# Optimization experiments

Hardware: AMD Instinct MI355X
Metric: run time of the kernel (lower is better)

The kernel has to match this reference:

```python
import jax, jax.numpy as jnp
import numpy as np

N_NODES = 512
STATE_DIM = 16
MESSAGE_DIM = 32
HID_MSG = 64
HID_RO = 64
N_STEPS = 5


def setup_inputs() -> dict:
    key = jax.random.key(0)
    ks = jax.random.split(key, 16)
    s, m, hm, hr = STATE_DIM, MESSAGE_DIM, HID_MSG, HID_RO
    gru_in = s + m
    k_gru = 1.0 / np.sqrt(s)
    inp = {
        'J': jax.random.normal(ks[0], (N_NODES, N_NODES), jnp.float32),
        'b': jax.random.normal(ks[1], (N_NODES,), jnp.float32),
        # message MLP (torch init: weight ~ N(0, 0.1), bias = 0)
        'W1': 0.1 * jax.random.normal(ks[2], (hm, 2 * s + 3), jnp.float32),
        'b1': jnp.zeros((hm,), jnp.float32),
        'W2': 0.1 * jax.random.normal(ks[3], (hm, hm), jnp.float32),
        'b2': jnp.zeros((hm,), jnp.float32),
        'W3': 0.1 * jax.random.normal(ks[4], (m, hm), jnp.float32),
        'b3': jnp.zeros((m,), jnp.float32),
        # GRUCell params (torch default: U(-1/sqrt(hidden), 1/sqrt(hidden)))
        'W_ih': jax.random.uniform(ks[5], (3 * s, gru_in), jnp.float32, -k_gru, k_gru),
        'b_ih': jnp.zeros((3 * s,), jnp.float32),
        'W_hh': jax.random.uniform(ks[6], (3 * s, s), jnp.float32, -k_gru, k_gru),
        'b_hh': jnp.zeros((3 * s,), jnp.float32),
        # readout MLP
        'Wr1': 0.1 * jax.random.normal(ks[7], (hr, s), jnp.float32),
        'br1': jnp.zeros((hr,), jnp.float32),
        'Wr2': 0.1 * jax.random.normal(ks[8], (hr, hr), jnp.float32),
        'br2': jnp.zeros((hr,), jnp.float32),
        'Wr3': 0.1 * jax.random.normal(ks[9], (2, hr), jnp.float32),
        'br3': jnp.zeros((2,), jnp.float32),
    }
    return inp


def _gru_cell(x, h, W_ih, b_ih, W_hh, b_hh):
    s = h.shape[-1]
    gi = x @ W_ih.T + b_ih  # (n, 3s)
    gh = h @ W_hh.T + b_hh  # (n, 3s)
    ir, iz, in_ = gi[:, :s], gi[:, s:2 * s], gi[:, 2 * s:]
    hr, hz, hn = gh[:, :s], gh[:, s:2 * s], gh[:, 2 * s:]
    r = jax.nn.sigmoid(ir + hr)
    z = jax.nn.sigmoid(iz + hz)
    n = jnp.tanh(in_ + r * hn)
    return (1.0 - z) * n + z * h


def reference(J, b, W1, b1, W2, b2, W3, b3, W_ih, b_ih, W_hh, b_hh,
              Wr1, br1, Wr2, br2, Wr3, br3):
    n = J.shape[0]
    s = W_hh.shape[1]
    # Split first message-MLP layer by input blocks [h_i | h_j | J_ij | b_i | b_j]
    # so we never materialize the (n, n, 2s+3) feature tensor.
    W1_hi = W1[:, :s]            # (hm, s)
    W1_hj = W1[:, s:2 * s]       # (hm, s)
    w_J = W1[:, 2 * s]           # (hm,)
    w_bi = W1[:, 2 * s + 1]      # (hm,)
    w_bj = W1[:, 2 * s + 2]      # (hm,)
    # static per-pair part of layer-1 preactivation: (n, n, hm)
    static1 = (J[:, :, None] * w_J
               + b[:, None, None] * w_bi
               + b[None, :, None] * w_bj
               + b1)

    h0 = jnp.zeros((n, s), jnp.float32)

    def step(h, _):
        pre = (h @ W1_hi.T)[:, None, :] + (h @ W1_hj.T)[None, :, :] + static1
        x = jax.nn.relu(pre)                      # (n, n, hm)
        x = jax.nn.relu(x @ W2.T + b2)            # (n, n, hm)
        msg = x @ W3.T + b3                       # (n, n, m)
        m_j = msg.sum(axis=0)                     # sum over i -> (n, m)
        gru_in = jnp.concatenate([h, m_j], axis=1)
        h_new = _gru_cell(gru_in, h, W_ih, b_ih, W_hh, b_hh)
        return h_new, None

    h, _ = jax.lax.scan(step, h0, None, length=N_STEPS)

    y = jax.nn.relu(h @ Wr1.T + br1)
    y = jax.nn.relu(y @ Wr2.T + br2)
    y = jax.nn.sigmoid(y @ Wr3.T + br3)           # (n, 2)
    y = y / jnp.sum(y, axis=1, keepdims=True)
    return y
```

## Files before the change

### kernel.cpp

```cpp
#include <hip/hip_runtime.h>
#include <hip/hip_bf16.h>

#define NN 512
#define NSTEPS 5

typedef __attribute__((ext_vector_type(8))) short short8;
typedef __attribute__((ext_vector_type(4))) float floatx4;

static __device__ __forceinline__ unsigned short f2bf(float f) {
    union { float f; unsigned u; } x; x.f = f;
    unsigned r = x.u + 0x7fffu + ((x.u >> 16) & 1u);
    return (unsigned short)(r >> 16);
}

static __device__ __forceinline__ unsigned pk2bf(float a, float b) {
    __hip_bfloat162 h = __float22bfloat162_rn(make_float2(a, b));
    return *reinterpret_cast<unsigned*>(&h);
}

__global__ void init_kernel(const float* __restrict__ J, const float* __restrict__ b,
                            const float* __restrict__ W1, const float* __restrict__ b1,
                            const float* __restrict__ W2,
                            float* __restrict__ Jt, float* __restrict__ aG, float* __restrict__ cG,
                            float* __restrict__ h0, float* __restrict__ wJ,
                            float* __restrict__ wbi, float* __restrict__ wbj,
                            float* __restrict__ W1hiT, float* __restrict__ W1hjT,
                            unsigned short* __restrict__ W2bf)
{
    int bx = blockIdx.x, tid = threadIdx.x;
    if (bx < 64) {
        __shared__ float tile[64][65];
        int ti = bx >> 3, tj = bx & 7;
        for (int p = 0; p < 16; ++p) {
            int e = p*256 + tid; int r = e >> 6, c = e & 63;
            tile[r][c] = J[(ti*64 + r)*512 + tj*64 + c];
        }
        __syncthreads();
        for (int p = 0; p < 16; ++p) {
            int e = p*256 + tid; int r = e >> 6, c = e & 63;
            Jt[(tj*64 + r)*512 + ti*64 + c] = tile[c][r];
        }
    } else if (bx < 96) {
        int gid = (bx - 64)*256 + tid;
        for (int p = 0; p < 4; ++p) {
            int idx = p*8192 + gid;
            int i = idx >> 6, o = idx & 63;
            aG[idx] = b[i] * W1[o*35 + 33];
        }
    } else if (bx < 128) {
        int gid = (bx - 96)*256 + tid;
        for (int p = 0; p < 4; ++p) {
            int idx = p*8192 + gid;
            int i = idx >> 6, o = idx & 63;
            cG[idx] = b[i] * W1[o*35 + 34] + b1[o];
        }
    } else if (bx == 128) {
        for (int p = 0; p < 16; ++p) {
            int flat = p*256 + tid;
            int jj = flat & 7;
            int lane = (flat >> 3) & 63;
            int tk = flat >> 9;
            int nt = tk >> 1, ks = tk & 1;
            int n = nt*16 + (lane & 15);
            int k = ks*32 + (lane >> 4)*8 + jj;
            W2bf[flat] = f2bf(W2[n*64 + k]);
        }
        if (tid < 64) {
            wJ[tid]  = W1[tid*35 + 32];
            wbi[tid] = W1[tid*35 + 33];
            wbj[tid] = W1[tid*35 + 34];
            #pragma unroll
            for (int s = 0; s < 16; ++s) {
                W1hiT[tid*16 + s] = W1[tid*35 + s];
                W1hjT[tid*16 + s] = W1[tid*35 + 16 + s];
            }
        }
    } else {
        for (int p = 0; p < 32; ++p) h0[p*256 + tid] = 0.f;
    }
}

__global__ __launch_bounds__(256) void edge_kernel(
    const float* __restrict__ Jt,
    const float* __restrict__ aIn, const float* __restrict__ cIn, const float* __restrict__ hIn,
    float* __restrict__ aOut, float* __restrict__ cOut, float* __restrict__ hOut,
    const unsigned short* __restrict__ W2bf, const float* __restrict__ wJ,
    const float* __restrict__ b2, const float* __restrict__ W3, const float* __restrict__ b3,
    const float* __restrict__ W_ih, const float* __restrict__ b_ih,
    const float* __restrict__ W_hh, const float* __restrict__ b_hh,
    const float* __restrict__ W1hiT, const float* __restrict__ W1hjT,
    const float* __restrict__ wbi, const float* __restrict__ wbj,
    const float* __restrict__ bvec, const float* __restrict__ b1,
    const float* __restrict__ Wr1, const float* __restrict__ br1,
    const float* __restrict__ Wr2, const float* __restrict__ br2,
    const float* __restrict__ Wr3, const float* __restrict__ br3,
    float* __restrict__ out, int last)
{
    const int j = blockIdx.x;
    const int tid = threadIdx.x;
    const int l = tid & 63, w = tid >> 6;
    const int m = l & 15, q = l >> 4;

    __shared__ float smWave[4][64];
    __shared__ float smMacc[64];
    __shared__ float smGin[48];
    __shared__ float smGi[48], smGh[48];
    __shared__ float smH[16];
    __shared__ float smY[64];
    __shared__ float smR[2];

    const floatx4* c4 = (const floatx4*)cIn;
    const floatx4* w4 = (const floatx4*)wJ;
    floatx4 cva = c4[j*16 + q*2],     cvb = c4[j*16 + q*2 + 1];
    floatx4 cvc = c4[j*16 + 8 + q*2], cvd = c4[j*16 + 8 + q*2 + 1];
    floatx4 wva = w4[q*2], wvb = w4[q*2+1], wvc = w4[8+q*2], wvd = w4[8+q*2+1];

    short8 bfw[4][2];
    {
        const short8* wb = (const short8*)W2bf;
        #pragma unroll
        for (int nt = 0; nt < 4; ++nt)
            #pragma unroll
            for (int ks = 0; ks < 2; ++ks)
                bfw[nt][ks] = wb[(nt*2 + ks)*64 + l];
    }
    float b2n[4];
    #pragma unroll
    for (int nt = 0; nt < 4; ++nt) b2n[nt] = b2[nt*16 + m];

    floatx4 acc[4];
    #pragma unroll
    for (int nt = 0; nt < 4; ++nt) acc[nt] = (floatx4){0.f,0.f,0.f,0.f};

    const floatx4* a4 = (const floatx4*)aIn;

    for (int c8 = 0; c8 < 8; ++c8) {
        int i = w*128 + c8*16 + m;
        float Jij = Jt[j*512 + i];
        floatx4 av0 = a4[i*16 + q*2],     av1 = a4[i*16 + q*2 + 1];
        floatx4 av2 = a4[i*16 + 8 + q*2], av3 = a4[i*16 + 8 + q*2 + 1];
        floatx4 x0, x1, x2, x3;
        #pragma unroll
        for (int e = 0; e < 4; ++e) {
            x0[e] = fmaxf(fmaf(Jij, wva[e], av0[e]) + cva[e], 0.f);
            x1[e] = fmaxf(fmaf(Jij, wvb[e], av1[e]) + cvb[e], 0.f);
            x2[e] = fmaxf(fmaf(Jij, wvc[e], av2[e]) + cvc[e], 0.f);
            x3[e] = fmaxf(fmaf(Jij, wvd[e], av3[e]) + cvd[e], 0.f);
        }
        union { short8 s; unsigned u[4]; } fa0, fa1;
        fa0.u[0] = pk2bf(x0[0], x0[1]); fa0.u[1] = pk2bf(x0[2], x0[3]);
        fa0.u[2] = pk2bf(x1[0], x1[1]); fa0.u[3] = pk2bf(x1[2], x1[3]);
        fa1.u[0] = pk2bf(x2[0], x2[1]); fa1.u[1] = pk2bf(x2[2], x2[3]);
        fa1.u[2] = pk2bf(x3[0], x3[1]); fa1.u[3] = pk2bf(x3[2], x3[3]);
        #pragma unroll
        for (int nt = 0; nt < 4; ++nt) {
            floatx4 d = {0.f,0.f,0.f,0.f};
            d = __builtin_amdgcn_mfma_f32_16x16x32_bf16(fa0.s, bfw[nt][0], d, 0, 0, 0);
            d = __builtin_amdgcn_mfma_f32_16x16x32_bf16(fa1.s, bfw[nt][1], d, 0, 0, 0);
            #pragma unroll
            for (int r = 0; r < 4; ++r)
                acc[nt][r] += fmaxf(d[r] + b2n[nt], 0.f);
        }
    }

    #pragma unroll
    for (int nt = 0; nt < 4; ++nt) {
        float v = acc[nt][0] + acc[nt][1] + acc[nt][2] + acc[nt][3];
        v += __shfl_xor(v, 16);
        v += __shfl_xor(v, 32);
        if (l < 16) smWave[w][nt*16 + l] = v;
    }
    if (tid < 16) smGin[tid] = hIn[j*16 + tid];
    __syncthreads();
    if (tid < 64) smMacc[tid] = smWave[0][tid] + smWave[1][tid] + smWave[2][tid] + smWave[3][tid];
    __syncthreads();

    {
        int o = tid >> 3, p = tid & 7;
        const floatx4* W3v = (const floatx4*)W3;
        floatx4 wv0 = W3v[o*16 + p*2], wv1 = W3v[o*16 + p*2 + 1];
        float part = 0.f;
        #pragma unroll
        for (int e = 0; e < 4; ++e) {
            part = fmaf(wv0[e], smMacc[p*8 + e], part);
            part = fmaf(wv1[e], smMacc[p*8 + 4 + e], part);
        }
        part += __shfl_xor(part, 1);
        part += __shfl_xor(part, 2);
        part += __shfl_xor(part, 4);
        if (p == 0) smGin[16 + o] = part + 512.f * b3[o];
    }
    __syncthreads();

    if (tid < 192) {
        int o = tid >> 2, p = tid & 3;
        const floatx4* Wv = (const floatx4*)W_ih;
        floatx4 w0 = Wv[o*12 + p*3], w1 = Wv[o*12 + p*3 + 1], w2 = Wv[o*12 + p*3 + 2];
        int k0 = p*12;
        float part = 0.f;
        #pragma unroll
        for (int e = 0; e < 4; ++e) {
            part = fmaf(w0[e], smGin[k0 + e], part);
            part = fmaf(w1[e], smGin[k0 + 4 + e], part);
            part = fmaf(w2[e], smGin[k0 + 8 + e], part);
        }
        part += __shfl_xor(part, 1);
        part += __shfl_xor(part, 2);
        if (p == 0) smGi[o] = part + b_ih[o];
    } else if (tid < 240) {
        int o = tid - 192;
        const floatx4* Wv = (const floatx4*)W_hh;
        floatx4 w0 = Wv[o*4], w1 = Wv[o*4+1], w2 = Wv[o*4+2], w3 = Wv[o*4+3];
        float s = b_hh[o];
        #pragma unroll
        for (int e = 0; e < 4; ++e) {
            s = fmaf(w0[e], smGin[e],      s);
            s = fmaf(w1[e], smGin[4 + e],  s);
            s = fmaf(w2[e], smGin[8 + e],  s);
            s = fmaf(w3[e], smGin[12 + e], s);
        }
        smGh[o] = s;
    }
    __syncthreads();

    if (tid < 16) {
        float r = 1.f / (1.f + __expf(-(smGi[tid] + smGh[tid])));
        float z = 1.f / (1.f + __expf(-(smGi[16+tid] + smGh[16+tid])));
        float n = tanhf(smGi[32+tid] + r * smGh[32+tid]);
        float hn = (1.f - z)*n + z*smGin[tid];
        hOut[j*16 + tid] = hn;
        smH[tid] = hn;
    }
    __syncthreads();

    if (!last) {
        if (tid < 128) {
            int o = tid & 63, sel = tid >> 6;
            const floatx4* Wv = (const floatx4*)(sel ? W1hjT : W1hiT);
            floatx4 w0 = Wv[o*4], w1 = Wv[o*4+1], w2 = Wv[o*4+2], w3 = Wv[o*4+3];
            float s = 0.f;
            #pragma unroll
            for (int e = 0; e < 4; ++e) {
                s = fmaf(w0[e], smH[e],      s);
                s = fmaf(w1[e], smH[4 + e],  s);
                s = fmaf(w2[e], smH[8 + e],  s);
                s = fmaf(w3[e], smH[12 + e], s);
            }
            if (sel == 0) aOut[j*64 + o] = s + bvec[j]*wbi[o];
            else          cOut[j*64 + o] = s + bvec[j]*wbj[o] + b1[o];
        }
    } else {
        if (tid < 64) {
            const floatx4* Wv = (const floatx4*)Wr1;
            floatx4 w0 = Wv[tid*4], w1 = Wv[tid*4+1], w2 = Wv[tid*4+2], w3 = Wv[tid*4+3];
            float s = br1[tid];
            #pragma unroll
            for (int e = 0; e < 4; ++e) {
                s = fmaf(w0[e], smH[e],      s);
                s = fmaf(w1[e], smH[4 + e],  s);
                s = fmaf(w2[e], smH[8 + e],  s);
                s = fmaf(w3[e], smH[12 + e], s);
            }
            smY[tid] = fmaxf(s, 0.f);
        }
        __syncthreads();
        {
            int o = tid >> 2, p = tid & 3;
            const floatx4* Wv = (const floatx4*)Wr2;
            floatx4 w0 = Wv[o*16 + p*4],     w1 = Wv[o*16 + p*4 + 1];
            floatx4 w2 = Wv[o*16 + p*4 + 2], w3 = Wv[o*16 + p*4 + 3];
            int k0 = p*16;
            float part = 0.f;
            #pragma unroll
            for (int e = 0; e < 4; ++e) {
                part = fmaf(w0[e], smY[k0 + e],      part);
                part = fmaf(w1[e], smY[k0 + 4 + e],  part);
                part = fmaf(w2[e], smY[k0 + 8 + e],  part);
                part = fmaf(w3[e], smY[k0 + 12 + e], part);
            }
            part += __shfl_xor(part, 1);
            part += __shfl_xor(part, 2);
            __syncthreads();
            if (p == 0) smY[o] = fmaxf(part + br2[o], 0.f);
        }
        __syncthreads();
        if (tid < 128) {
            int ot = tid >> 6, p = tid & 63;
            float part = Wr3[ot*64 + p] * smY[p];
            part += __shfl_xor(part, 1);
            part += __shfl_xor(part, 2);
            part += __shfl_xor(part, 4);
            part += __shfl_xor(part, 8);
            part += __shfl_xor(part, 16);
            part += __shfl_xor(part, 32);
            if (p == 0) smR[ot] = part + br3[ot];
        }
        __syncthreads();
        if (tid == 0) {
            float e0 = 1.f/(1.f + __expf(-smR[0]));
            float e1 = 1.f/(1.f + __expf(-smR[1]));
            float t = e0 + e1;
            out[j*2]     = e0/t;
            out[j*2 + 1] = e1/t;
        }
    }
}

extern "C" void kernel_launch(void* const* d_in, const int* in_sizes, int n_in,
                              void* d_out, int out_size, void* d_ws, size_t ws_size,
                              hipStream_t stream)
{
    const float* J    = (const float*)d_in[0];
    const float* b    = (const float*)d_in[1];
    const float* W1   = (const float*)d_in[2];
    const float* b1   = (const float*)d_in[3];
    const float* W2   = (const float*)d_in[4];
    const float* b2   = (const float*)d_in[5];
    const float* W3   = (const float*)d_in[6];
    const float* b3   = (const float*)d_in[7];
    const float* W_ih = (const float*)d_in[8];
    const float* b_ih = (const float*)d_in[9];
    const float* W_hh = (const float*)d_in[10];
    const float* b_hh = (const float*)d_in[11];
    const float* Wr1  = (const float*)d_in[12];
    const float* br1  = (const float*)d_in[13];
    const float* Wr2  = (const float*)d_in[14];
    const float* br2  = (const float*)d_in[15];
    const float* Wr3  = (const float*)d_in[16];
    const float* br3  = (const float*)d_in[17];
    float* out = (float*)d_out;

    float* ws   = (float*)d_ws;
    float* Jt   = ws;
    float* aG0  = Jt + 262144;
    float* aG1  = aG0 + 32768;
    float* cG0  = aG1 + 32768;
    float* cG1  = cG0 + 32768;
    float* hA   = cG1 + 32768;
    float* hB   = hA + 8192;
    float* wJ   = hB + 8192;
    float* wbi  = wJ + 64;
    float* wbj  = wbi + 64;
    float* W1hiT = wbj + 64;
    float* W1hjT = W1hiT + 1024;
    unsigned short* W2bf = (unsigned short*)(W1hjT + 1024);

    hipLaunchKernelGGL(init_kernel, dim3(130), dim3(256), 0, stream,
                       J, b, W1, b1, W2, Jt, aG0, cG0, hA, wJ, wbi, wbj, W1hiT, W1hjT, W2bf);

    float* aIn = aG0; float* aOut = aG1;
    float* cIn = cG0; float* cOut = cG1;
    float* hI  = hA;  float* hO  = hB;
    for (int t = 0; t < NSTEPS; ++t) {
        hipLaunchKernelGGL(edge_kernel, dim3(512), dim3(256), 0, stream,
            Jt, aIn, cIn, hI, aOut, cOut, hO, W2bf, wJ, b2, W3, b3,
            W_ih, b_ih, W_hh, b_hh, W1hiT, W1hjT, wbi, wbj, b, b1,
            Wr1, br1, Wr2, br2, Wr3, br3, out, (t == NSTEPS-1) ? 1 : 0);
        float* tmp;
        tmp = aIn; aIn = aOut; aOut = tmp;
        tmp = cIn; cIn = cOut; cOut = tmp;
        tmp = hI;  hI  = hO;  hO  = tmp;
    }
}
```

Measured before the change: 155.0 us.

## Fuse init and all GNN steps into one cooperative persistent kernel with grid sync

Replaces the init kernel plus five per-step edge kernel launches with a single cooperative kernel of 256 blocks, each handling two destination nodes. Steps are separated by grid.sync(), so launch overhead and inter-kernel gaps go away. The J column, W2 weights in bf16 and the W1 slices now stay in registers or shared memory across all steps instead of being reloaded each launch, and the J transpose is dropped. The trade-off is the cost of grid-wide barriers and fewer blocks; the old multi-launch path remains as a fallback if the cooperative launch fails.

```diff
diff --git a/kernel.cpp b/kernel.cpp
--- a/kernel.cpp
+++ b/kernel.cpp
@@ -1,5 +1,8 @@
 #include <hip/hip_runtime.h>
 #include <hip/hip_bf16.h>
+#include <hip/hip_cooperative_groups.h>
+
+namespace cg = cooperative_groups;
 
 #define NN 512
 #define NSTEPS 5
@@ -16,6 +19,287 @@
 static __device__ __forceinline__ unsigned pk2bf(float a, float b) {
     __hip_bfloat162 h = __float22bfloat162_rn(make_float2(a, b));
     return *reinterpret_cast<unsigned*>(&h);
+}
+
+__global__ __launch_bounds__(512, 2) void fused2_kernel(
+    const float* __restrict__ J, const float* __restrict__ b,
+    const float* __restrict__ W1, const float* __restrict__ b1,
+    const float* __restrict__ W2, const float* __restrict__ b2,
+    const float* __restrict__ W3, const float* __restrict__ b3,
+    const float* __restrict__ W_ih, const float* __restrict__ b_ih,
+    const float* __restrict__ W_hh, const float* __restrict__ b_hh,
+    const float* __restrict__ Wr1, const float* __restrict__ br1,
+    const float* __restrict__ Wr2, const float* __restrict__ br2,
+    const float* __restrict__ Wr3, const float* __restrict__ br3,
+    float* __restrict__ aBuf0, float* __restrict__ aBuf1,
+    float* __restrict__ out)
+{
+    cg::grid_group grid = cg::this_grid();
+    const int tid = threadIdx.x;
+    const int nd = tid >> 8;
+    const int tl = tid & 255;
+    const int j  = blockIdx.x * 2 + nd;
+    const int l  = tid & 63, w4 = tl >> 6;
+    const int m  = l & 15,  q  = l >> 4;
+
+    __shared__ float smW1hi[64][16], smW1hj[64][16];
+    __shared__ float smC[2][64], smAbias[2][64], smCbias[2][64];
+    __shared__ float smWave[2][4][64], smMacc[2][64];
+    __shared__ float smGin[2][48], smGi[2][48], smGh[2][48];
+    __shared__ float smH[2][16], smY[2][64], smR[2][2];
+
+    if (tid < 64) {
+        const float* w1r = W1 + tid*35;
+        #pragma unroll
+        for (int s = 0; s < 16; ++s) {
+            smW1hi[tid][s] = w1r[s];
+            smW1hj[tid][s] = w1r[16 + s];
+        }
+    }
+    if (tid < 128) {
+        int nd0 = tid >> 6, o = tid & 63;
+        int j0 = blockIdx.x*2 + nd0;
+        float bj0 = b[j0];
+        const float* w1r = W1 + o*35;
+        float ab = bj0 * w1r[33];
+        smAbias[nd0][o] = ab;
+        float cb = bj0 * w1r[34] + b1[o];
+        smCbias[nd0][o] = cb;
+        smC[nd0][o] = cb;
+        aBuf0[j0*64 + o] = ab;
+    }
+    if (tid >= 128 && tid < 160) {
+        int nd0 = (tid - 128) >> 4, o = (tid - 128) & 15;
+        smH[nd0][o] = 0.f;
+    }
+
+    float Jr[8];
+    #pragma unroll
+    for (int c8 = 0; c8 < 8; ++c8)
+        Jr[c8] = J[(w4*128 + c8*16 + m)*512 + j];
+
+    floatx4 wva, wvb, wvc, wvd;
+    #pragma unroll
+    for (int e = 0; e < 4; ++e) {
+        wva[e] = W1[(q*8 + e)*35 + 32];
+        wvb[e] = W1[(q*8 + 4 + e)*35 + 32];
+        wvc[e] = W1[(32 + q*8 + e)*35 + 32];
+        wvd[e] = W1[(32 + q*8 + 4 + e)*35 + 32];
+    }
+
+    short8 bfw[4][2];
+    #pragma unroll
+    for (int nt = 0; nt < 4; ++nt) {
+        #pragma unroll
+        for (int ks = 0; ks < 2; ++ks) {
+            union { short8 s; unsigned short us[8]; } tpk;
+            int n = nt*16 + m;
+            #pragma unroll
+            for (int jj = 0; jj < 8; ++jj)
+                tpk.us[jj] = f2bf(W2[n*64 + ks*32 + q*8 + jj]);
+            bfw[nt][ks] = tpk.s;
+        }
+    }
+    float b2n[4];
+    #pragma unroll
+    for (int nt = 0; nt < 4; ++nt) b2n[nt] = b2[nt*16 + m];
+
+    grid.sync();
+
+    float* aIn = aBuf0;
+    float* aOut = aBuf1;
+
+    for (int t = 0; t < NSTEPS; ++t) {
+        const int last = (t == NSTEPS - 1);
+
+        floatx4 cva, cvb, cvc, cvd;
+        #pragma unroll
+        for (int e = 0; e < 4; ++e) {
+            cva[e] = smC[nd][q*8 + e];
+            cvb[e] = smC[nd][q*8 + 4 + e];
+            cvc[e] = smC[nd][32 + q*8 + e];
+            cvd[e] = smC[nd][32 + q*8 + 4 + e];
+        }
+
+        floatx4 acc[4];
+        #pragma unroll
+        for (int nt = 0; nt < 4; ++nt) acc[nt] = (floatx4){0.f,0.f,0.f,0.f};
+
+        const floatx4* a4 = (const floatx4*)aIn;
+
+        for (int c8 = 0; c8 < 8; ++c8) {
+            int i = w4*128 + c8*16 + m;
+            float Jij = Jr[c8];
+            floatx4 av0 = a4[i*16 + q*2],     av1 = a4[i*16 + q*2 + 1];
+            floatx4 av2 = a4[i*16 + 8 + q*2], av3 = a4[i*16 + 8 + q*2 + 1];
+            floatx4 x0, x1, x2, x3;
+            #pragma unroll
+            for (int e = 0; e < 4; ++e) {
+                x0[e] = fmaxf(fmaf(Jij, wva[e], av0[e]) + cva[e], 0.f);
+                x1[e] = fmaxf(fmaf(Jij, wvb[e], av1[e]) + cvb[e], 0.f);
+                x2[e] = fmaxf(fmaf(Jij, wvc[e], av2[e]) + cvc[e], 0.f);
+                x3[e] = fmaxf(fmaf(Jij, wvd[e], av3[e]) + cvd[e], 0.f);
+            }
+            union { short8 s; unsigned u[4]; } fa0, fa1;
+            fa0.u[0] = pk2bf(x0[0], x0[1]); fa0.u[1] = pk2bf(x0[2], x0[3]);
+            fa0.u[2] = pk2bf(x1[0], x1[1]); fa0.u[3] = pk2bf(x1[2], x1[3]);
+            fa1.u[0] = pk2bf(x2[0], x2[1]); fa1.u[1] = pk2bf(x2[2], x2[3]);
+            fa1.u[2] = pk2bf(x3[0], x3[1]); fa1.u[3] = pk2bf(x3[2], x3[3]);
+            #pragma unroll
+            for (int nt = 0; nt < 4; ++nt) {
+                floatx4 d = {0.f,0.f,0.f,0.f};
+                d = __builtin_amdgcn_mfma_f32_16x16x32_bf16(fa0.s, bfw[nt][0], d, 0, 0, 0);
+                d = __builtin_amdgcn_mfma_f32_16x16x32_bf16(fa1.s, bfw[nt][1], d, 0, 0, 0);
+                #pragma unroll
+                for (int r = 0; r < 4; ++r)
+                    acc[nt][r] += fmaxf(d[r] + b2n[nt], 0.f);
+            }
+        }
+
+        #pragma unroll
+        for (int nt = 0; nt < 4; ++nt) {
+            float v = acc[nt][0] + acc[nt][1] + acc[nt][2] + acc[nt][3];
+            v += __shfl_xor(v, 16);
+            v += __shfl_xor(v, 32);
+            if (l < 16) smWave[nd][w4][nt*16 + l] = v;
+        }
+        if (tl < 16) smGin[nd][tl] = smH[nd][tl];
+        __syncthreads();
+        if (tl < 64) smMacc[nd][tl] = smWave[nd][0][tl] + smWave[nd][1][tl]
+                                    + smWave[nd][2][tl] + smWave[nd][3][tl];
+        __syncthreads();
+
+        {
+            int o = tl >> 3, p = tl & 7;
+            const floatx4* W3v = (const floatx4*)W3;
+            floatx4 wv0 = W3v[o*16 + p*2], wv1 = W3v[o*16 + p*2 + 1];
+            float part = 0.f;
+            #pragma unroll
+            for (int e = 0; e < 4; ++e) {
+                part = fmaf(wv0[e], smMacc[nd][p*8 + e], part);
+                part = fmaf(wv1[e], smMacc[nd][p*8 + 4 + e], part);
+            }
+            part += __shfl_xor(part, 1);
+            part += __shfl_xor(part, 2);
+            part += __shfl_xor(part, 4);
+            if (p == 0) smGin[nd][16 + o] = part + 512.f * b3[o];
+        }
+        __syncthreads();
+
+        if (tl < 192) {
+            int o = tl >> 2, p = tl & 3;
+            const floatx4* Wv = (const floatx4*)W_ih;
+            floatx4 w0 = Wv[o*12 + p*3], w1 = Wv[o*12 + p*3 + 1], w2 = Wv[o*12 + p*3 + 2];
+            int k0 = p*12;
+            float part = 0.f;
+            #pragma unroll
+            for (int e = 0; e < 4; ++e) {
+                part = fmaf(w0[e], smGin[nd][k0 + e], part);
+                part = fmaf(w1[e], smGin[nd][k0 + 4 + e], part);
+                part = fmaf(w2[e], smGin[nd][k0 + 8 + e], part);
+            }
+            part += __shfl_xor(part, 1);
+            part += __shfl_xor(part, 2);
+            if (p == 0) smGi[nd][o] = part + b_ih[o];
+        } else if (tl < 240) {
+            int o = tl - 192;
+            const floatx4* Wv = (const floatx4*)W_hh;
+            floatx4 w0 = Wv[o*4], w1 = Wv[o*4+1], w2 = Wv[o*4+2], w3 = Wv[o*4+3];
+            float s2 = b_hh[o];
+            #pragma unroll
+            for (int e = 0; e < 4; ++e) {
+                s2 = fmaf(w0[e], smGin[nd][e],      s2);
+                s2 = fmaf(w1[e], smGin[nd][4 + e],  s2);
+                s2 = fmaf(w2[e], smGin[nd][8 + e],  s2);
+                s2 = fmaf(w3[e], smGin[nd][12 + e], s2);
+            }
+            smGh[nd][o] = s2;
+        }
+        __syncthreads();
+
+        if (tl < 16) {
+            float r = 1.f / (1.f + __expf(-(smGi[nd][tl] + smGh[nd][tl])));
+            float z = 1.f / (1.f + __expf(-(smGi[nd][16+tl] + smGh[nd][16+tl])));
+            float n = tanhf(smGi[nd][32+tl] + r * smGh[nd][32+tl]);
+            float hn = (1.f - z)*n + z*smGin[nd][tl];
+            smH[nd][tl] = hn;
+        }
+        __syncthreads();
+
+        if (!last) {
+            if (tl < 128) {
+                int o = tl & 63, sel = tl >> 6;
+                const floatx4* Wv = (const floatx4*)(sel ? &smW1hj[0][0] : &smW1hi[0][0]);
+                floatx4 w0 = Wv[o*4], w1 = Wv[o*4+1], w2 = Wv[o*4+2], w3 = Wv[o*4+3];
+                float s = 0.f;
+                #pragma unroll
+                for (int e = 0; e < 4; ++e) {
+                    s = fmaf(w0[e], smH[nd][e],      s);
+                    s = fmaf(w1[e], smH[nd][4 + e],  s);
+                    s = fmaf(w2[e], smH[nd][8 + e],  s);
+                    s = fmaf(w3[e], smH[nd][12 + e], s);
+                }
+                if (sel == 0) aOut[j*64 + o] = s + smAbias[nd][o];
+                else          smC[nd][o] = s + smCbias[nd][o];
+            }
+            grid.sync();
+            float* tmp = aIn; aIn = aOut; aOut = tmp;
+        } else {
+            if (tl < 64) {
+                const floatx4* Wv = (const floatx4*)Wr1;
+                floatx4 w0 = Wv[tl*4], w1 = Wv[tl*4+1], w2 = Wv[tl*4+2], w3 = Wv[tl*4+3];
+                float s = br1[tl];
+                #pragma unroll
+                for (int e = 0; e < 4; ++e) {
+                    s = fmaf(w0[e], smH[nd][e],      s);
+                    s = fmaf(w1[e], smH[nd][4 + e],  s);
+                    s = fmaf(w2[e], smH[nd][8 + e],  s);
+                    s = fmaf(w3[e], smH[nd][12 + e], s);
+                }
+                smY[nd][tl] = fmaxf(s, 0.f);
+            }
+            __syncthreads();
+            {
+                int o = tl >> 2, p = tl & 3;
+                const floatx4* Wv = (const floatx4*)Wr2;
+                floatx4 w0 = Wv[o*16 + p*4],     w1 = Wv[o*16 + p*4 + 1];
+                floatx4 w2 = Wv[o*16 + p*4 + 2], w3 = Wv[o*16 + p*4 + 3];
+                int k0 = p*16;
+                float part = 0.f;
+                #pragma unroll
+                for (int e = 0; e < 4; ++e) {
+                    part = fmaf(w0[e], smY[nd][k0 + e],      part);
+                    part = fmaf(w1[e], smY[nd][k0 + 4 + e],  part);
+                    part = fmaf(w2[e], smY[nd][k0 + 8 + e],  part);
+                    part = fmaf(w3[e], smY[nd][k0 + 12 + e], part);
+                }
+                part += __shfl_xor(part, 1);
+                part += __shfl_xor(part, 2);
+                __syncthreads();
+                if (p == 0) smY[nd][o] = fmaxf(part + br2[o], 0.f);
+            }
+            __syncthreads();
+            if (tl < 128) {
+                int ot = tl >> 6, p = tl & 63;
+                float part = Wr3[ot*64 + p] * smY[nd][p];
+                part += __shfl_xor(part, 1);
+                part += __shfl_xor(part, 2);
+                part += __shfl_xor(part, 4);
+                part += __shfl_xor(part, 8);
+                part += __shfl_xor(part, 16);
+                part += __shfl_xor(part, 32);
+                if (p == 0) smR[nd][ot] = part + br3[ot];
+            }
+            __syncthreads();
+            if (tl == 0) {
+                float e0 = 1.f/(1.f + __expf(-smR[nd][0]));
+                float e1 = 1.f/(1.f + __expf(-smR[nd][1]));
+                float tsum = e0 + e1;
+                out[j*2]     = e0/tsum;
+                out[j*2 + 1] = e1/tsum;
+            }
+        }
+    }
 }
 
 __global__ void init_kernel(const float* __restrict__ J, const float* __restrict__ b,
@@ -328,10 +612,35 @@
     const float* br2  = (const float*)d_in[15];
     const float* Wr3  = (const float*)d_in[16];
     const float* br3  = (const float*)d_in[17];
-    float* out = (float*)d_out;
-
-    float* ws   = (float*)d_ws;
-    float* Jt   = ws;
+    float* outp = (float*)d_out;
+
+    float* ws = (float*)d_ws;
+
+    static int coop_attr = -1;
+    if (coop_attr < 0) {
+        int v = 0;
+        if (hipDeviceGetAttribute(&v, hipDeviceAttributeCooperativeLaunch, 0) != hipSuccess) v = 0;
+        coop_attr = v;
+    }
+
+    float* aBuf0 = ws;
+    float* aBuf1 = ws + 32768;
+
+    hipError_t lerr = hipErrorUnknown;
+    if (coop_attr) {
+        void* args[] = {
+            (void*)&J, (void*)&b, (void*)&W1, (void*)&b1, (void*)&W2, (void*)&b2,
+            (void*)&W3, (void*)&b3, (void*)&W_ih, (void*)&b_ih, (void*)&W_hh, (void*)&b_hh,
+            (void*)&Wr1, (void*)&br1, (void*)&Wr2, (void*)&br2, (void*)&Wr3, (void*)&br3,
+            (void*)&aBuf0, (void*)&aBuf1, (void*)&outp
+        };
+        lerr = hipLaunchCooperativeKernel(reinterpret_cast<void*>(fused2_kernel),
+                                          dim3(NN/2), dim3(512), args, 0, stream);
+    }
+    if (lerr == hipSuccess) return;
+    (void)hipGetLastError();
+
+    float* Jt   = ws + 65536;
     float* aG0  = Jt + 262144;
     float* aG1  = aG0 + 32768;
     float* cG0  = aG1 + 32768;
@@ -355,7 +664,7 @@
         hipLaunchKernelGGL(edge_kernel, dim3(512), dim3(256), 0, stream,
             Jt, aIn, cIn, hI, aOut, cOut, hO, W2bf, wJ, b2, W3, b3,
             W_ih, b_ih, W_hh, b_hh, W1hiT, W1hjT, wbi, wbj, b, b1,
-            Wr1, br1, Wr2, br2, Wr3, br3, out, (t == NSTEPS-1) ? 1 : 0);
+            Wr1, br1, Wr2, br2, Wr3, br3, outp, (t == NSTEPS-1) ? 1 : 0);
         float* tmp;
         tmp = aIn; aIn = aOut; aOut = tmp;
         tmp = cIn; cIn = cOut; cOut = tmp;
```

Measured after the change: 304.0 us. +96.1%, slower.

## Fuse init and all GRU steps into one persistent kernel with flag sync

Applied to the files above, without the earlier changes.

Replaces the init kernel and the five per-step launches with a single persistent kernel of 256 blocks, each handling two nodes. Blocks exchange the per-node layer-1 'a' vectors through per-step global buffers and spin on padded per-node flags rather than relying on kernel boundaries. The c vector and hidden state stay in shared memory. J is read column-wise directly into registers instead of through a transpose, and W2 is converted to bf16 in every block. The aim is to remove launch overhead and the full grid barrier between steps. In exchange it relies on all 256 blocks being co-resident and on correct memory ordering for the flag spin-waits, and it adds polling cost plus redundant per-block weight preparation.

```diff
diff --git a/kernel.cpp b/kernel.cpp
--- a/kernel.cpp
+++ b/kernel.cpp
@@ -3,6 +3,7 @@
 
 #define NN 512
 #define NSTEPS 5
+#define FSTR 32
 
 typedef __attribute__((ext_vector_type(8))) short short8;
 typedef __attribute__((ext_vector_type(4))) float floatx4;
@@ -18,290 +19,319 @@
     return *reinterpret_cast<unsigned*>(&h);
 }
 
-__global__ void init_kernel(const float* __restrict__ J, const float* __restrict__ b,
-                            const float* __restrict__ W1, const float* __restrict__ b1,
-                            const float* __restrict__ W2,
-                            float* __restrict__ Jt, float* __restrict__ aG, float* __restrict__ cG,
-                            float* __restrict__ h0, float* __restrict__ wJ,
-                            float* __restrict__ wbi, float* __restrict__ wbj,
-                            float* __restrict__ W1hiT, float* __restrict__ W1hjT,
-                            unsigned short* __restrict__ W2bf)
-{
-    int bx = blockIdx.x, tid = threadIdx.x;
-    if (bx < 64) {
-        __shared__ float tile[64][65];
-        int ti = bx >> 3, tj = bx & 7;
-        for (int p = 0; p < 16; ++p) {
-            int e = p*256 + tid; int r = e >> 6, c = e & 63;
-            tile[r][c] = J[(ti*64 + r)*512 + tj*64 + c];
-        }
-        __syncthreads();
-        for (int p = 0; p < 16; ++p) {
-            int e = p*256 + tid; int r = e >> 6, c = e & 63;
-            Jt[(tj*64 + r)*512 + ti*64 + c] = tile[c][r];
-        }
-    } else if (bx < 96) {
-        int gid = (bx - 64)*256 + tid;
-        for (int p = 0; p < 4; ++p) {
-            int idx = p*8192 + gid;
-            int i = idx >> 6, o = idx & 63;
-            aG[idx] = b[i] * W1[o*35 + 33];
-        }
-    } else if (bx < 128) {
-        int gid = (bx - 96)*256 + tid;
-        for (int p = 0; p < 4; ++p) {
-            int idx = p*8192 + gid;
-            int i = idx >> 6, o = idx & 63;
-            cG[idx] = b[i] * W1[o*35 + 34] + b1[o];
-        }
-    } else if (bx == 128) {
-        for (int p = 0; p < 16; ++p) {
-            int flat = p*256 + tid;
-            int jj = flat & 7;
-            int lane = (flat >> 3) & 63;
-            int tk = flat >> 9;
-            int nt = tk >> 1, ks = tk & 1;
-            int n = nt*16 + (lane & 15);
-            int k = ks*32 + (lane >> 4)*8 + jj;
-            W2bf[flat] = f2bf(W2[n*64 + k]);
-        }
-        if (tid < 64) {
-            wJ[tid]  = W1[tid*35 + 32];
-            wbi[tid] = W1[tid*35 + 33];
-            wbj[tid] = W1[tid*35 + 34];
-            #pragma unroll
-            for (int s = 0; s < 16; ++s) {
-                W1hiT[tid*16 + s] = W1[tid*35 + s];
-                W1hjT[tid*16 + s] = W1[tid*35 + 16 + s];
-            }
-        }
-    } else {
-        for (int p = 0; p < 32; ++p) h0[p*256 + tid] = 0.f;
-    }
-}
-
-__global__ __launch_bounds__(256) void edge_kernel(
-    const float* __restrict__ Jt,
-    const float* __restrict__ aIn, const float* __restrict__ cIn, const float* __restrict__ hIn,
-    float* __restrict__ aOut, float* __restrict__ cOut, float* __restrict__ hOut,
-    const unsigned short* __restrict__ W2bf, const float* __restrict__ wJ,
-    const float* __restrict__ b2, const float* __restrict__ W3, const float* __restrict__ b3,
+__global__ __launch_bounds__(512, 2) void fused3_kernel(
+    const float* __restrict__ J, const float* __restrict__ b,
+    const float* __restrict__ W1, const float* __restrict__ b1,
+    const float* __restrict__ W2, const float* __restrict__ b2,
+    const float* __restrict__ W3, const float* __restrict__ b3,
     const float* __restrict__ W_ih, const float* __restrict__ b_ih,
     const float* __restrict__ W_hh, const float* __restrict__ b_hh,
-    const float* __restrict__ W1hiT, const float* __restrict__ W1hjT,
-    const float* __restrict__ wbi, const float* __restrict__ wbj,
-    const float* __restrict__ bvec, const float* __restrict__ b1,
     const float* __restrict__ Wr1, const float* __restrict__ br1,
     const float* __restrict__ Wr2, const float* __restrict__ br2,
     const float* __restrict__ Wr3, const float* __restrict__ br3,
-    float* __restrict__ out, int last)
+    float* __restrict__ aP, int* __restrict__ flag,
+    float* __restrict__ out)
 {
-    const int j = blockIdx.x;
     const int tid = threadIdx.x;
-    const int l = tid & 63, w = tid >> 6;
-    const int m = l & 15, q = l >> 4;
-
-    __shared__ float smWave[4][64];
-    __shared__ float smMacc[64];
-    __shared__ float smGin[48];
-    __shared__ float smGi[48], smGh[48];
-    __shared__ float smH[16];
-    __shared__ float smY[64];
-    __shared__ float smR[2];
-
-    const floatx4* c4 = (const floatx4*)cIn;
-    const floatx4* w4 = (const floatx4*)wJ;
-    floatx4 cva = c4[j*16 + q*2],     cvb = c4[j*16 + q*2 + 1];
-    floatx4 cvc = c4[j*16 + 8 + q*2], cvd = c4[j*16 + 8 + q*2 + 1];
-    floatx4 wva = w4[q*2], wvb = w4[q*2+1], wvc = w4[8+q*2], wvd = w4[8+q*2+1];
+    const int bid = blockIdx.x;
+    const int nd = tid >> 8;
+    const int tl = tid & 255;
+    const int j  = bid * 2 + nd;
+    const int l  = tid & 63, w4 = tl >> 6;
+    const int m  = l & 15,  q  = l >> 4;
+
+    __shared__ float smW1hi[64][16], smW1hj[64][16];
+    __shared__ float smC[2][64], smAbias[2][64], smCbias[2][64];
+    __shared__ float smWave[2][4][64], smMacc[2][64];
+    __shared__ float smGin[2][48], smGi[2][48], smGh[2][48];
+    __shared__ float smH[2][16], smY[2][64], smR[2][2];
+
+    __builtin_amdgcn_fence(__ATOMIC_ACQUIRE, "agent");
+
+    if (tid < 128) {
+        int nd0 = tid >> 6, o = tid & 63;
+        int j0 = bid*2 + nd0;
+        float bj0 = b[j0];
+        const float* w1r = W1 + o*35;
+        float ab = bj0 * w1r[33];
+        smAbias[nd0][o] = ab;
+        float cb = bj0 * w1r[34] + b1[o];
+        smCbias[nd0][o] = cb;
+        smC[nd0][o] = cb;
+        __hip_atomic_store(&aP[32768 + j0*64 + o], ab,
+                           __ATOMIC_RELAXED, __HIP_MEMORY_SCOPE_AGENT);
+    }
+    if (tid < 128) {
+        asm volatile("s_waitcnt vmcnt(0)" ::: "memory");
+        if ((tid & 63) == 0)
+            __hip_atomic_store(&flag[(bid*2 + (tid >> 6))*FSTR], 1,
+                               __ATOMIC_RELAXED, __HIP_MEMORY_SCOPE_AGENT);
+    }
+    if (tid >= 128 && tid < 160) {
+        int nd0 = (tid - 128) >> 4, o = (tid - 128) & 15;
+        smH[nd0][o] = 0.f;
+    }
+    if (tid < 64) {
+        const float* w1r = W1 + tid*35;
+        #pragma unroll
+        for (int s0 = 0; s0 < 16; ++s0) {
+            smW1hi[tid][s0] = w1r[s0];
+            smW1hj[tid][s0] = w1r[16 + s0];
+        }
+    }
+
+    float Jr[8];
+    #pragma unroll
+    for (int c8 = 0; c8 < 8; ++c8)
+        Jr[c8] = J[(w4*128 + c8*16 + m)*512 + j];
+
+    floatx4 wva, wvb, wvc, wvd;
+    #pragma unroll
+    for (int e = 0; e < 4; ++e) {
+        wva[e] = W1[(q*8 + e)*35 + 32];
+        wvb[e] = W1[(q*8 + 4 + e)*35 + 32];
+        wvc[e] = W1[(32 + q*8 + e)*35 + 32];
+        wvd[e] = W1[(32 + q*8 + 4 + e)*35 + 32];
+    }
 
     short8 bfw[4][2];
-    {
-        const short8* wb = (const short8*)W2bf;
-        #pragma unroll
-        for (int nt = 0; nt < 4; ++nt)
-            #pragma unroll
-            for (int ks = 0; ks < 2; ++ks)
-                bfw[nt][ks] = wb[(nt*2 + ks)*64 + l];
+    #pragma unroll
+    for (int nt = 0; nt < 4; ++nt) {
+        #pragma unroll
+        for (int ks = 0; ks < 2; ++ks) {
+            union { short8 s; unsigned short us[8]; } tpk;
+            int n = nt*16 + m;
+            #pragma unroll
+            for (int jj = 0; jj < 8; ++jj)
+                tpk.us[jj] = f2bf(W2[n*64 + ks*32 + q*8 + jj]);
+            bfw[nt][ks] = tpk.s;
+        }
     }
     float b2n[4];
     #pragma unroll
     for (int nt = 0; nt < 4; ++nt) b2n[nt] = b2[nt*16 + m];
 
-    floatx4 acc[4];
-    #pragma unroll
-    for (int nt = 0; nt < 4; ++nt) acc[nt] = (floatx4){0.f,0.f,0.f,0.f};
-
-    const floatx4* a4 = (const floatx4*)aIn;
-
-    for (int c8 = 0; c8 < 8; ++c8) {
-        int i = w*128 + c8*16 + m;
-        float Jij = Jt[j*512 + i];
-        floatx4 av0 = a4[i*16 + q*2],     av1 = a4[i*16 + q*2 + 1];
-        floatx4 av2 = a4[i*16 + 8 + q*2], av3 = a4[i*16 + 8 + q*2 + 1];
-        floatx4 x0, x1, x2, x3;
+    __syncthreads();
+
+    for (int t = 0; t < NSTEPS; ++t) {
+        const int last = (t == NSTEPS - 1);
+        const int s = t + 1;
+
+        floatx4 cva, cvb, cvc, cvd;
         #pragma unroll
         for (int e = 0; e < 4; ++e) {
-            x0[e] = fmaxf(fmaf(Jij, wva[e], av0[e]) + cva[e], 0.f);
-            x1[e] = fmaxf(fmaf(Jij, wvb[e], av1[e]) + cvb[e], 0.f);
-            x2[e] = fmaxf(fmaf(Jij, wvc[e], av2[e]) + cvc[e], 0.f);
-            x3[e] = fmaxf(fmaf(Jij, wvd[e], av3[e]) + cvd[e], 0.f);
-        }
-        union { short8 s; unsigned u[4]; } fa0, fa1;
-        fa0.u[0] = pk2bf(x0[0], x0[1]); fa0.u[1] = pk2bf(x0[2], x0[3]);
-        fa0.u[2] = pk2bf(x1[0], x1[1]); fa0.u[3] = pk2bf(x1[2], x1[3]);
-        fa1.u[0] = pk2bf(x2[0], x2[1]); fa1.u[1] = pk2bf(x2[2], x2[3]);
-        fa1.u[2] = pk2bf(x3[0], x3[1]); fa1.u[3] = pk2bf(x3[2], x3[3]);
+            cva[e] = smC[nd][q*8 + e];
+            cvb[e] = smC[nd][q*8 + 4 + e];
+            cvc[e] = smC[nd][32 + q*8 + e];
+            cvd[e] = smC[nd][32 + q*8 + 4 + e];
+        }
+
+        {
+            const int rbase = w4*128 + m;
+            for (;;) {
+                int f0 = __hip_atomic_load(&flag[(rbase +   0)*FSTR], __ATOMIC_RELAXED, __HIP_MEMORY_SCOPE_AGENT);
+                int f1 = __hip_atomic_load(&flag[(rbase +  16)*FSTR], __ATOMIC_RELAXED, __HIP_MEMORY_SCOPE_AGENT);
+                int f2 = __hip_atomic_load(&flag[(rbase +  32)*FSTR], __ATOMIC_RELAXED, __HIP_MEMORY_SCOPE_AGENT);
+                int f3 = __hip_atomic_load(&flag[(rbase +  48)*FSTR], __ATOMIC_RELAXED, __HIP_MEMORY_SCOPE_AGENT);
+                int f4 = __hip_atomic_load(&flag[(rbase +  64)*FSTR], __ATOMIC_RELAXED, __HIP_MEMORY_SCOPE_AGENT);
+                int f5 = __hip_atomic_load(&flag[(rbase +  80)*FSTR], __ATOMIC_RELAXED, __HIP_MEMORY_SCOPE_AGENT);
+                int f6 = __hip_atomic_load(&flag[(rbase +  96)*FSTR], __ATOMIC_RELAXED, __HIP_MEMORY_SCOPE_AGENT);
+                int f7 = __hip_atomic_load(&flag[(rbase + 112)*FSTR], __ATOMIC_RELAXED, __HIP_MEMORY_SCOPE_AGENT);
+                int mn = min(min(min(f0, f1), min(f2, f3)),
+                             min(min(f4, f5), min(f6, f7)));
+                if (mn >= s) break;
+                __builtin_amdgcn_s_sleep(1);
+            }
+        }
+        asm volatile("" ::: "memory");
+
+        floatx4 acc[4];
+        #pragma unroll
+        for (int nt = 0; nt < 4; ++nt) acc[nt] = (floatx4){0.f,0.f,0.f,0.f};
+
+        const floatx4* a4 = (const floatx4*)(aP + (size_t)s*32768);
+
+        for (int c8 = 0; c8 < 8; ++c8) {
+            int i = w4*128 + c8*16 + m;
+            float Jij = Jr[c8];
+            floatx4 av0 = a4[i*16 + q*2],     av1 = a4[i*16 + q*2 + 1];
+            floatx4 av2 = a4[i*16 + 8 + q*2], av3 = a4[i*16 + 8 + q*2 + 1];
+            floatx4 x0, x1, x2, x3;
+            #pragma unroll
+            for (int e = 0; e < 4; ++e) {
+                x0[e] = fmaxf(fmaf(Jij, wva[e], av0[e]) + cva[e], 0.f);
+                x1[e] = fmaxf(fmaf(Jij, wvb[e], av1[e]) + cvb[e], 0.f);
+                x2[e] = fmaxf(fmaf(Jij, wvc[e], av2[e]) + cvc[e], 0.f);
+                x3[e] = fmaxf(fmaf(Jij, wvd[e], av3[e]) + cvd[e], 0.f);
+            }
+            union { short8 s; unsigned u[4]; } fa0, fa1;
+            fa0.u[0] = pk2bf(x0[0], x0[1]); fa0.u[1] = pk2bf(x0[2], x0[3]);
+            fa0.u[2] = pk2bf(x1[0], x1[1]); fa0.u[3] = pk2bf(x1[2], x1[3]);
+            fa1.u[0] = pk2bf(x2[0], x2[1]); fa1.u[1] = pk2bf(x2[2], x2[3]);
+            fa1.u[2] = pk2bf(x3[0], x3[1]); fa1.u[3] = pk2bf(x3[2], x3[3]);
+            #pragma unroll
+            for (int nt = 0; nt < 4; ++nt) {
+                floatx4 d = {0.f,0.f,0.f,0.f};
+                d = __builtin_amdgcn_mfma_f32_16x16x32_bf16(fa0.s, bfw[nt][0], d, 0, 0, 0);
+                d = __builtin_amdgcn_mfma_f32_16x16x32_bf16(fa1.s, bfw[nt][1], d, 0, 0, 0);
+                #pragma unroll
+                for (int r = 0; r < 4; ++r)
+                    acc[nt][r] += fmaxf(d[r] + b2n[nt], 0.f);
+            }
+        }
+
         #pragma unroll
         for (int nt = 0; nt < 4; ++nt) {
-            floatx4 d = {0.f,0.f,0.f,0.f};
-            d = __builtin_amdgcn_mfma_f32_16x16x32_bf16(fa0.s, bfw[nt][0], d, 0, 0, 0);
-            d = __builtin_amdgcn_mfma_f32_16x16x32_bf16(fa1.s, bfw[nt][1], d, 0, 0, 0);
-            #pragma unroll
-            for (int r = 0; r < 4; ++r)
-                acc[nt][r] += fmaxf(d[r] + b2n[nt], 0.f);
-        }
-    }
-
-    #pragma unroll
-    for (int nt = 0; nt < 4; ++nt) {
-        float v = acc[nt][0] + acc[nt][1] + acc[nt][2] + acc[nt][3];
-        v += __shfl_xor(v, 16);
-        v += __shfl_xor(v, 32);
-        if (l < 16) smWave[w][nt*16 + l] = v;
-    }
-    if (tid < 16) smGin[tid] = hIn[j*16 + tid];
-    __syncthreads();
-    if (tid < 64) smMacc[tid] = smWave[0][tid] + smWave[1][tid] + smWave[2][tid] + smWave[3][tid];
-    __syncthreads();
-
-    {
-        int o = tid >> 3, p = tid & 7;
-        const floatx4* W3v = (const floatx4*)W3;
-        floatx4 wv0 = W3v[o*16 + p*2], wv1 = W3v[o*16 + p*2 + 1];
-        float part = 0.f;
-        #pragma unroll
-        for (int e = 0; e < 4; ++e) {
-            part = fmaf(wv0[e], smMacc[p*8 + e], part);
-            part = fmaf(wv1[e], smMacc[p*8 + 4 + e], part);
-        }
-        part += __shfl_xor(part, 1);
-        part += __shfl_xor(part, 2);
-        part += __shfl_xor(part, 4);
-        if (p == 0) smGin[16 + o] = part + 512.f * b3[o];
-    }
-    __syncthreads();
-
-    if (tid < 192) {
-        int o = tid >> 2, p = tid & 3;
-        const floatx4* Wv = (const floatx4*)W_ih;
-        floatx4 w0 = Wv[o*12 + p*3], w1 = Wv[o*12 + p*3 + 1], w2 = Wv[o*12 + p*3 + 2];
-        int k0 = p*12;
-        float part = 0.f;
-        #pragma unroll
-        for (int e = 0; e < 4; ++e) {
-            part = fmaf(w0[e], smGin[k0 + e], part);
-            part = fmaf(w1[e], smGin[k0 + 4 + e], part);
-            part = fmaf(w2[e], smGin[k0 + 8 + e], part);
-        }
-        part += __shfl_xor(part, 1);
-        part += __shfl_xor(part, 2);
-        if (p == 0) smGi[o] = part + b_ih[o];
-    } else if (tid < 240) {
-        int o = tid - 192;
-        const floatx4* Wv = (const floatx4*)W_hh;
-        floatx4 w0 = Wv[o*4], w1 = Wv[o*4+1], w2 = Wv[o*4+2], w3 = Wv[o*4+3];
-        float s = b_hh[o];
-        #pragma unroll
-        for (int e = 0; e < 4; ++e) {
-            s = fmaf(w0[e], smGin[e],      s);
-            s = fmaf(w1[e], smGin[4 + e],  s);
-            s = fmaf(w2[e], smGin[8 + e],  s);
-            s = fmaf(w3[e], smGin[12 + e], s);
-        }
-        smGh[o] = s;
-    }
-    __syncthreads();
-
-    if (tid < 16) {
-        float r = 1.f / (1.f + __expf(-(smGi[tid] + smGh[tid])));
-        float z = 1.f / (1.f + __expf(-(smGi[16+tid] + smGh[16+tid])));
-        float n = tanhf(smGi[32+tid] + r * smGh[32+tid]);
-        float hn = (1.f - z)*n + z*smGin[tid];
-        hOut[j*16 + tid] = hn;
-        smH[tid] = hn;
-    }
-    __syncthreads();
-
-    if (!last) {
-        if (tid < 128) {
-            int o = tid & 63, sel = tid >> 6;
-            const floatx4* Wv = (const floatx4*)(sel ? W1hjT : W1hiT);
-            floatx4 w0 = Wv[o*4], w1 = Wv[o*4+1], w2 = Wv[o*4+2], w3 = Wv[o*4+3];
-            float s = 0.f;
+            float v = acc[nt][0] + acc[nt][1] + acc[nt][2] + acc[nt][3];
+            v += __shfl_xor(v, 16);
+            v += __shfl_xor(v, 32);
+            if (l < 16) smWave[nd][w4][nt*16 + l] = v;
+        }
+        if (tl < 16) smGin[nd][tl] = smH[nd][tl];
+        __syncthreads();
+        if (tl < 64) smMacc[nd][tl] = smWave[nd][0][tl] + smWave[nd][1][tl]
+                                    + smWave[nd][2][tl] + smWave[nd][3][tl];
+        __syncthreads();
+
+        {
+            int o = tl >> 3, p = tl & 7;
+            const floatx4* W3v = (const floatx4*)W3;
+            floatx4 wv0 = W3v[o*16 + p*2], wv1 = W3v[o*16 + p*2 + 1];
+            float part = 0.f;
             #pragma unroll
             for (int e = 0; e < 4; ++e) {
-                s = fmaf(w0[e], smH[e],      s);
-                s = fmaf(w1[e], smH[4 + e],  s);
-                s = fmaf(w2[e], smH[8 + e],  s);
-                s = fmaf(w3[e], smH[12 + e], s);
-            }
-            if (sel == 0) aOut[j*64 + o] = s + bvec[j]*wbi[o];
-            else          cOut[j*64 + o] = s + bvec[j]*wbj[o] + b1[o];
-        }
-    } else {
-        if (tid < 64) {
-            const floatx4* Wv = (const floatx4*)Wr1;
-            floatx4 w0 = Wv[tid*4], w1 = Wv[tid*4+1], w2 = Wv[tid*4+2], w3 = Wv[tid*4+3];
-            float s = br1[tid];
-            #pragma unroll
-            for (int e = 0; e < 4; ++e) {
-                s = fmaf(w0[e], smH[e],      s);
-                s = fmaf(w1[e], smH[4 + e],  s);
-                s = fmaf(w2[e], smH[8 + e],  s);
-                s = fmaf(w3[e], smH[12 + e], s);
-            }
-            smY[tid] = fmaxf(s, 0.f);
-        }
-        __syncthreads();
-        {
-            int o = tid >> 2, p = tid & 3;
-            const floatx4* Wv = (const floatx4*)Wr2;
-            floatx4 w0 = Wv[o*16 + p*4],     w1 = Wv[o*16 + p*4 + 1];
-            floatx4 w2 = Wv[o*16 + p*4 + 2], w3 = Wv[o*16 + p*4 + 3];
-            int k0 = p*16;
-            float part = 0.f;
-            #pragma unroll
-            for (int e = 0; e < 4; ++e) {
-                part = fmaf(w0[e], smY[k0 + e],      part);
-                part = fmaf(w1[e], smY[k0 + 4 + e],  part);
-                part = fmaf(w2[e], smY[k0 + 8 + e],  part);
-                part = fmaf(w3[e], smY[k0 + 12 + e], part);
-            }
-            part += __shfl_xor(part, 1);
-            part += __shfl_xor(part, 2);
-            __syncthreads();
-            if (p == 0) smY[o] = fmaxf(part + br2[o], 0.f);
-        }
-        __syncthreads();
-        if (tid < 128) {
-            int ot = tid >> 6, p = tid & 63;
-            float part = Wr3[ot*64 + p] * smY[p];
+                part = fmaf(wv0[e], smMacc[nd][p*8 + e], part);
+                part = fmaf(wv1[e], smMacc[nd][p*8 + 4 + e], part);
+            }
             part += __shfl_xor(part, 1);
             part += __shfl_xor(part, 2);
             part += __shfl_xor(part, 4);
-            part += __shfl_xor(part, 8);
-            part += __shfl_xor(part, 16);
-            part += __shfl_xor(part, 32);
-            if (p == 0) smR[ot] = part + br3[ot];
-        }
-        __syncthreads();
-        if (tid == 0) {
-            float e0 = 1.f/(1.f + __expf(-smR[0]));
-            float e1 = 1.f/(1.f + __expf(-smR[1]));
-            float t = e0 + e1;
-            out[j*2]     = e0/t;
-            out[j*2 + 1] = e1/t;
+            if (p == 0) smGin[nd][16 + o] = part + 512.f * b3[o];
+        }
+        __syncthreads();
+
+        if (tl < 192) {
+            int o = tl >> 2, p = tl & 3;
+            const floatx4* Wv = (const floatx4*)W_ih;
+            floatx4 w0 = Wv[o*12 + p*3], w1 = Wv[o*12 + p*3 + 1], w2 = Wv[o*12 + p*3 + 2];
+            int k0 = p*12;
+            float part = 0.f;
+            #pragma unroll
+            for (int e = 0; e < 4; ++e) {
+                part = fmaf(w0[e], smGin[nd][k0 + e], part);
+                part = fmaf(w1[e], smGin[nd][k0 + 4 + e], part);
+                part = fmaf(w2[e], smGin[nd][k0 + 8 + e], part);
+            }
+            part += __shfl_xor(part, 1);
+            part += __shfl_xor(part, 2);
+            if (p == 0) smGi[nd][o] = part + b_ih[o];
+        } else if (tl < 240) {
+            int o = tl - 192;
+            const floatx4* Wv = (const floatx4*)W_hh;
+            floatx4 w0 = Wv[o*4], w1 = Wv[o*4+1], w2 = Wv[o*4+2], w3 = Wv[o*4+3];
+            float s2 = b_hh[o];
+            #pragma unroll
+            for (int e = 0; e < 4; ++e) {
+                s2 = fmaf(w0[e], smGin[nd][e],      s2);
+                s2 = fmaf(w1[e], smGin[nd][4 + e],  s2);
+                s2 = fmaf(w2[e], smGin[nd][8 + e],  s2);
+                s2 = fmaf(w3[e], smGin[nd][12 + e], s2);
+            }
+            smGh[nd][o] = s2;
+        }
+        __syncthreads();
+
+        if (tl < 16) {
+            float r = 1.f / (1.f + __expf(-(smGi[nd][tl] + smGh[nd][tl])));
+            float z = 1.f / (1.f + __expf(-(smGi[nd][16+tl] + smGh[nd][16+tl])));
+            float n = tanhf(smGi[nd][32+tl] + r * smGh[nd][32+tl]);
+            float hn = (1.f - z)*n + z*smGin[nd][tl];
+            smH[nd][tl] = hn;
+        }
+        __syncthreads();
+
+        if (!last) {
+            if (tl < 128) {
+                int o = tl & 63, sel = tl >> 6;
+                const floatx4* Wv = (const floatx4*)(sel ? &smW1hj[0][0] : &smW1hi[0][0]);
+                floatx4 w0 = Wv[o*4], w1 = Wv[o*4+1], w2 = Wv[o*4+2], w3 = Wv[o*4+3];
+                float sacc = 0.f;
+                #pragma unroll
+                for (int e = 0; e < 4; ++e) {
+                    sacc = fmaf(w0[e], smH[nd][e],      sacc);
+                    sacc = fmaf(w1[e], smH[nd][4 + e],  sacc);
+                    sacc = fmaf(w2[e], smH[nd][8 + e],  sacc);
+                    sacc = fmaf(w3[e], smH[nd][12 + e], sacc);
+                }
+                if (sel == 0) {
+                    __hip_atomic_store(&aP[(size_t)(s+1)*32768 + j*64 + o],
+                                       sacc + smAbias[nd][o],
+                                       __ATOMIC_RELAXED, __HIP_MEMORY_SCOPE_AGENT);
+                } else {
+                    smC[nd][o] = sacc + smCbias[nd][o];
+                }
+            }
+            if (tl < 64) {
+                asm volatile("s_waitcnt vmcnt(0)" ::: "memory");
+                if (tl == 0)
+                    __hip_atomic_store(&flag[j*FSTR], s + 1,
+                                       __ATOMIC_RELAXED, __HIP_MEMORY_SCOPE_AGENT);
+            }
+            __syncthreads();
+        } else {
+            if (tl < 64) {
+                const floatx4* Wv = (const floatx4*)Wr1;
+                floatx4 w0 = Wv[tl*4], w1 = Wv[tl*4+1], w2 = Wv[tl*4+2], w3 = Wv[tl*4+3];
+                float sacc = br1[tl];
+                #pragma unroll
+                for (int e = 0; e < 4; ++e) {
+                    sacc = fmaf(w0[e], smH[nd][e],      sacc);
+                    sacc = fmaf(w1[e], smH[nd][4 + e],  sacc);
+                    sacc = fmaf(w2[e], smH[nd][8 + e],  sacc);
+                    sacc = fmaf(w3[e], smH[nd][12 + e], sacc);
+                }
+                smY[nd][tl] = fmaxf(sacc, 0.f);
+            }
+            __syncthreads();
+            {
+                int o = tl >> 2, p = tl & 3;
+                const floatx4* Wv = (const floatx4*)Wr2;
+                floatx4 w0 = Wv[o*16 + p*4],     w1 = Wv[o*16 + p*4 + 1];
+                floatx4 w2 = Wv[o*16 + p*4 + 2], w3 = Wv[o*16 + p*4 + 3];
+                int k0 = p*16;
+                float part = 0.f;
+                #pragma unroll
+                for (int e = 0; e < 4; ++e) {
+                    part = fmaf(w0[e], smY[nd][k0 + e],      part);
+                    part = fmaf(w1[e], smY[nd][k0 + 4 + e],  part);
+                    part = fmaf(w2[e], smY[nd][k0 + 8 + e],  part);
+                    part = fmaf(w3[e], smY[nd][k0 + 12 + e], part);
+                }
+                part += __shfl_xor(part, 1);
+                part += __shfl_xor(part, 2);
+                __syncthreads();
+                if (p == 0) smY[nd][o] = fmaxf(part + br2[o], 0.f);
+            }
+            __syncthreads();
+            if (tl < 128) {
+                int ot = tl >> 6, p = tl & 63;
+                float part = Wr3[ot*64 + p] * smY[nd][p];
+                part += __shfl_xor(part, 1);
+                part += __shfl_xor(part, 2);
+                part += __shfl_xor(part, 4);
+                part += __shfl_xor(part, 8);
+                part += __shfl_xor(part, 16);
+                part += __shfl_xor(part, 32);
+                if (p == 0) smR[nd][ot] = part + br3[ot];
+            }
+            __syncthreads();
+            if (tl == 0) {
+                float e0 = 1.f/(1.f + __expf(-smR[nd][0]));
+                float e1 = 1.f/(1.f + __expf(-smR[nd][1]));
+                float tsum = e0 + e1;
+                out[j*2]     = e0/tsum;
+                out[j*2 + 1] = e1/tsum;
+            }
         }
     }
 }
@@ -328,37 +358,16 @@
     const float* br2  = (const float*)d_in[15];
     const float* Wr3  = (const float*)d_in[16];
     const float* br3  = (const float*)d_in[17];
-    float* out = (float*)d_out;
-
-    float* ws   = (float*)d_ws;
-    float* Jt   = ws;
-    float* aG0  = Jt + 262144;
-    float* aG1  = aG0 + 32768;
-    float* cG0  = aG1 + 32768;
-    float* cG1  = cG0 + 32768;
-    float* hA   = cG1 + 32768;
-    float* hB   = hA + 8192;
-    float* wJ   = hB + 8192;
-    float* wbi  = wJ + 64;
-    float* wbj  = wbi + 64;
-    float* W1hiT = wbj + 64;
-    float* W1hjT = W1hiT + 1024;
-    unsigned short* W2bf = (unsigned short*)(W1hjT + 1024);
-
-    hipLaunchKernelGGL(init_kernel, dim3(130), dim3(256), 0, stream,
-                       J, b, W1, b1, W2, Jt, aG0, cG0, hA, wJ, wbi, wbj, W1hiT, W1hjT, W2bf);
-
-    float* aIn = aG0; float* aOut = aG1;
-    float* cIn = cG0; float* cOut = cG1;
-    float* hI  = hA;  float* hO  = hB;
-    for (int t = 0; t < NSTEPS; ++t) {
-        hipLaunchKernelGGL(edge_kernel, dim3(512), dim3(256), 0, stream,
-            Jt, aIn, cIn, hI, aOut, cOut, hO, W2bf, wJ, b2, W3, b3,
-            W_ih, b_ih, W_hh, b_hh, W1hiT, W1hjT, wbi, wbj, b, b1,
-            Wr1, br1, Wr2, br2, Wr3, br3, out, (t == NSTEPS-1) ? 1 : 0);
-        float* tmp;
-        tmp = aIn; aIn = aOut; aOut = tmp;
-        tmp = cIn; cIn = cOut; cOut = tmp;
-        tmp = hI;  hI  = hO;  hO  = tmp;
-    }
+    float* outp = (float*)d_out;
+
+    float* ws = (float*)d_ws;
+    float* aP    = ws;
+    int*   flags = (int*)(ws + 6*32768);
+    const size_t FLAG_BYTES = 512u * FSTR * sizeof(int);
+
+    hipMemsetAsync((void*)flags, 0, FLAG_BYTES, stream);
+
+    hipLaunchKernelGGL(fused3_kernel, dim3(NN/2), dim3(512), 0, stream,
+        J, b, W1, b1, W2, b2, W3, b3, W_ih, b_ih, W_hh, b_hh,
+        Wr1, br1, Wr2, br2, Wr3, br3, aP, flags, outp);
 }
```

After: 171.6 us. 1.11x slower.
